# Kernel optimization log

Hardware: AMD Instinct MI355X
Metric: run time of the kernel (lower is better)

The kernel has to match this reference:

```python
import jax, jax.numpy as jnp
import numpy as np
import math

D = 128          # cfg.hiden_features_size
P0, P1 = 32, 32  # cfg.patch_size
T = 1.0          # default forward arg t


def _temporal_pe():
    # pe_k[i, :] = cat_j [sin(arg(t,i,j)), cos(arg(t,i,j))], i in [0,P1), j in [0,P0//2)
    i = jnp.arange(P1, dtype=jnp.float32)[:, None]          # [P1, 1]
    j = jnp.arange(P0 // 2, dtype=jnp.float32)[None, :]     # [1, P0//2]
    arg = T * jnp.pi * i / (1000.0 ** (2.0 * j / D))         # [P1, P0//2]
    pe = jnp.stack([jnp.sin(arg), jnp.cos(arg)], axis=-1)    # [P1, P0//2, 2]
    return pe.reshape(P1, P0)                                # [P1, P0]


def setup_inputs() -> dict:
    key = jax.random.key(0)
    kx, kw, kb = jax.random.split(key, 3)
    N, S = 128, P0 * P1
    x = jax.random.normal(kx, (N, S, D), dtype=jnp.float32)
    W = jax.random.normal(kw, (3 * D, D), dtype=jnp.float32) * (1.0 / math.sqrt(D))
    b = jax.random.normal(kb, (3 * D,), dtype=jnp.float32) * 0.01
    return {"x": x, "W": W, "b": b}


def reference(x, W, b):
    N, S, d = x.shape  # S = P0*P1, d = D
    # temporal positional encoding: multiply in spatial layout [N, P0, P1, d]
    pe = _temporal_pe()                                  # [P1, P0] (broadcast over x's [P0, P1])
    xs = x.reshape(N, P0, P1, d) * pe[None, :, :, None]
    xs = xs.reshape(N, S, d)
    # fused qkv projection: Linear(d, 3d)
    h = jnp.einsum('nsd,fd->nsf', xs, W) + b             # [N, S, 3d]
    # quirky split: view(N, S*d, 3) interleaves features in groups of 3
    qkv = h.reshape(N, S * d, 3)
    q, k, v = qkv[..., 0], qkv[..., 1], qkv[..., 2]      # each [N, S*d]
    # attention over the batch dimension: scores are [N, N]
    scores = (q @ k.T) / math.sqrt(d)
    attn = jax.nn.softmax(scores, axis=-1)
    return attn @ v                                      # [N, S*d]
```

## Files before the change

kernel.cpp:

```cpp
#include <hip/hip_runtime.h>
#include <math.h>

#define N_   128
#define S_   1024
#define D_   128
#define SD_  (S_ * D_)

#define WSP_PLANE 49152
#define NREP 16
#define SB   2
#define GRID_SC (S_ / SB)

typedef __attribute__((ext_vector_type(8))) short bf16x8;
typedef __attribute__((ext_vector_type(4))) short bf16x4;
typedef __attribute__((ext_vector_type(4))) float f32x4;
#define MFMA16 __builtin_amdgcn_mfma_f32_16x16x32_bf16

__device__ __forceinline__ float pe_scale(int s) {
    int i = s >> 5;
    int c = s & 31;
    double rexp = pow(1000.0, -(double)(c & ~1) / 128.0);
    double arg = M_PI * (double)i * rexp;
    return (float)((c & 1) ? cos(arg) : sin(arg));
}

__device__ __forceinline__ unsigned short bf16_rn(float f) {
    unsigned int u = __float_as_uint(f);
    u += 0x7fff + ((u >> 16) & 1);
    return (unsigned short)(u >> 16);
}
__device__ __forceinline__ float bf16_f(unsigned short h) {
    return __uint_as_float(((unsigned int)h) << 16);
}
__device__ __forceinline__ void split2(float f, unsigned short& h, unsigned short& l) {
    h = bf16_rn(f);
    l = bf16_rn(f - bf16_f(h));
}

__device__ __forceinline__ void load_split8(const float* p, float scale,
                                            bf16x8& hi, bf16x8& lo) {
    float4 u0 = *(const float4*)(p);
    float4 u1 = *(const float4*)(p + 4);
    unsigned short h[8], l[8];
    split2(u0.x * scale, h[0], l[0]); split2(u0.y * scale, h[1], l[1]);
    split2(u0.z * scale, h[2], l[2]); split2(u0.w * scale, h[3], l[3]);
    split2(u1.x * scale, h[4], l[4]); split2(u1.y * scale, h[5], l[5]);
    split2(u1.z * scale, h[6], l[6]); split2(u1.w * scale, h[7], l[7]);
    hi = bf16x8{(short)h[0],(short)h[1],(short)h[2],(short)h[3],
                (short)h[4],(short)h[5],(short)h[6],(short)h[7]};
    lo = bf16x8{(short)l[0],(short)l[1],(short)l[2],(short)l[3],
                (short)l[4],(short)l[5],(short)l[6],(short)l[7]};
}

__global__ __launch_bounds__(256) void k_prep(const float* __restrict__ W,
                                              unsigned short* __restrict__ Wsp,
                                              float* __restrict__ peT) {
    const int idx = blockIdx.x * 256 + threadIdx.x;
    if (idx < S_) peT[idx] = pe_scale(idx);
    const int rg = idx >> 7;
    const int d  = idx & 127;
    const int p  = rg % 3;
    const int r  = rg / 3;
    const int rc = r >> 5, m = r & 31;
    const int ks = d >> 5, quad = (d >> 3) & 3, j = d & 7;
    unsigned short h, l;
    split2(W[idx], h, l);
    const size_t off = (size_t)((((p * 4 + rc) * 4 + ks) * 4 + quad) * 32 + m) * 8 + j;
    Wsp[off] = h;
    Wsp[off + WSP_PLANE] = l;
}

__global__ __launch_bounds__(512, 4) void k_scores(const float* __restrict__ x,
                                                   const unsigned short* __restrict__ Wsp,
                                                   const float* __restrict__ b,
                                                   const float* __restrict__ peT,
                                                   float* __restrict__ sc,
                                                   int store_mode) {
    __shared__ unsigned short qk[4][128 * 40];
    __shared__ float bl[384];

    const int t    = threadIdx.x;
    const int lane = t & 63;
    const int wv   = t >> 6;
    const int lid  = lane & 15;
    const int quad = lane >> 4;

    if (t < 128) { bl[t] = b[t]; bl[t + 128] = b[t + 128]; bl[t + 256] = b[t + 256]; }
    __syncthreads();

    const f32x4 fzero = {0.f, 0.f, 0.f, 0.f};
    f32x4 sacc[8];
#pragma unroll
    for (int j = 0; j < 8; ++j) sacc[j] = fzero;

    for (int ss = 0; ss < SB; ++ss) {
        const int s = blockIdx.x * SB + ss;
        const float ps = peT[s];

        bf16x8 xh[4], xl[4];
        {
            const int row = wv * 16 + lid;
            const float* xp = x + (size_t)row * SD_ + (size_t)s * D_;
#pragma unroll
            for (int ks = 0; ks < 4; ++ks)
                load_split8(xp + ks * 32 + quad * 8, ps, xh[ks], xl[ks]);
        }

        for (int rc = 0; rc < 4; ++rc) {
            for (int p = 0; p < 2; ++p) {
                f32x4 pacc[2];
                pacc[0] = fzero; pacc[1] = fzero;
#pragma unroll
                for (int ks = 0; ks < 4; ++ks) {
                    const unsigned short* wb =
                        Wsp + (size_t)(((p * 4 + rc) * 4 + ks) * 4 + quad) * 256;
                    bf16x8 wh[2], wl[2];
#pragma unroll
                    for (int mt = 0; mt < 2; ++mt) {
                        wh[mt] = *(const bf16x8*)(wb + (mt * 16 + lid) * 8);
                        wl[mt] = *(const bf16x8*)(wb + WSP_PLANE + (mt * 16 + lid) * 8);
                    }
#pragma unroll
                    for (int mt = 0; mt < 2; ++mt) {
                        pacc[mt] = MFMA16(wh[mt], xh[ks], pacc[mt], 0, 0, 0);
                        pacc[mt] = MFMA16(wh[mt], xl[ks], pacc[mt], 0, 0, 0);
                        pacc[mt] = MFMA16(wl[mt], xh[ks], pacc[mt], 0, 0, 0);
                    }
                }
#pragma unroll
                for (int mt = 0; mt < 2; ++mt) {
                    const int n = wv * 16 + lid;
                    unsigned short hh[4], ll[4];
#pragma unroll
                    for (int r = 0; r < 4; ++r) {
                        const int rg = rc * 32 + mt * 16 + quad * 4 + r;
                        float qv = pacc[mt][r] + bl[3 * rg + p];
                        split2(qv, hh[r], ll[r]);
                    }
                    bf16x4 hv = {(short)hh[0], (short)hh[1], (short)hh[2], (short)hh[3]};
                    bf16x4 lv = {(short)ll[0], (short)ll[1], (short)ll[2], (short)ll[3]};
                    *(bf16x4*)&qk[p * 2 + 0][n * 40 + mt * 16 + quad * 4] = hv;
                    *(bf16x4*)&qk[p * 2 + 1][n * 40 + mt * 16 + quad * 4] = lv;
                }
            }
            __syncthreads();
            {
                const int row = wv * 16 + lid;
                bf16x8 qh = *(const bf16x8*)&qk[0][row * 40 + quad * 8];
                bf16x8 ql = *(const bf16x8*)&qk[1][row * 40 + quad * 8];
#pragma unroll
                for (int ntp = 0; ntp < 8; ++ntp) {
                    const int krow = ntp * 16 + lid;
                    bf16x8 kh = *(const bf16x8*)&qk[2][krow * 40 + quad * 8];
                    bf16x8 kl = *(const bf16x8*)&qk[3][krow * 40 + quad * 8];
                    sacc[ntp] = MFMA16(qh, kh, sacc[ntp], 0, 0, 0);
                    sacc[ntp] = MFMA16(qh, kl, sacc[ntp], 0, 0, 0);
                    sacc[ntp] = MFMA16(ql, kh, sacc[ntp], 0, 0, 0);
                }
            }
            __syncthreads();
        }
    }

    float* rep = sc + (store_mode ? (size_t)blockIdx.x * (N_ * N_)
                                  : (size_t)(blockIdx.x & (NREP - 1)) * (N_ * N_));
#pragma unroll
    for (int ntp = 0; ntp < 8; ++ntp)
#pragma unroll
        for (int r = 0; r < 4; ++r) {
            const int n  = wv * 16 + quad * 4 + r;
            const int np = ntp * 16 + lid;
            if (store_mode) rep[n * N_ + np] = sacc[ntp][r];
            else            atomicAdd(&rep[n * N_ + np], sacc[ntp][r]);
        }
}

__global__ __launch_bounds__(1024) void k_softmax(const float* __restrict__ sc, int R,
                                                  unsigned short* __restrict__ att2) {
    const int n  = blockIdx.x;
    const int t  = threadIdx.x;
    const int rg = t >> 5;
    const int c4 = (t & 31) * 4;

    float4 a = {0.f, 0.f, 0.f, 0.f};
    for (int rep = rg; rep < R; rep += 32) {
        const float4 p = *(const float4*)&sc[(size_t)rep * (N_ * N_) + n * N_ + c4];
        a.x += p.x; a.y += p.y; a.z += p.z; a.w += p.w;
    }
    __shared__ float tmp[32][128];
    *(float4*)&tmp[rg][c4] = a;
    __syncthreads();

    __shared__ float red[2];
    __shared__ float red2[2];

    float v = 0.f;
    if (t < 128) {
#pragma unroll
        for (int g = 0; g < 32; ++g) v += tmp[g][t];
        v *= 0.08838834764831845f;
    }

    float m = v;
#pragma unroll
    for (int o = 32; o > 0; o >>= 1) m = fmaxf(m, __shfl_xor(m, o));
    if (t < 128 && (t & 63) == 0) red[t >> 6] = m;
    __syncthreads();
    m = fmaxf(red[0], red[1]);

    float e = (t < 128) ? expf(v - m) : 0.f;
    float sum = e;
#pragma unroll
    for (int o = 32; o > 0; o >>= 1) sum += __shfl_xor(sum, o);
    if (t < 128 && (t & 63) == 0) red2[t >> 6] = sum;
    __syncthreads();
    sum = red2[0] + red2[1];

    if (t < 128) {
        const int ks = t >> 5, quad = (t >> 3) & 3, j = t & 7;
        att2[(size_t)(((ks * 4 + quad) * 128) + n) * 8 + j] = bf16_rn(e / sum);
    }
}

__global__ __launch_bounds__(256, 2) void k_out(const float* __restrict__ x,
                                                const unsigned short* __restrict__ Wsp,
                                                const float* __restrict__ b,
                                                const unsigned short* __restrict__ att2,
                                                const float* __restrict__ peT,
                                                float* __restrict__ out) {
    __shared__ unsigned short vT[128 * 136];
    __shared__ float bv[128];

    const int t    = threadIdx.x;
    const int lane = t & 63;
    const int wv   = t >> 6;
    const int lid  = lane & 15;
    const int quad = lane >> 4;
    const int s    = blockIdx.x;
    const float ps = peT[s];

    if (t < 128) bv[t] = b[3 * t + 2];
    __syncthreads();

    const f32x4 fzero = {0.f, 0.f, 0.f, 0.f};

    bf16x8 xh[2][4], xl[2][4];
#pragma unroll
    for (int mt = 0; mt < 2; ++mt) {
        const int row = (wv * 2 + mt) * 16 + lid;
        const float* xp = x + (size_t)row * SD_ + (size_t)s * D_;
#pragma unroll
        for (int ks = 0; ks < 4; ++ks)
            load_split8(xp + ks * 32 + quad * 8, ps, xh[mt][ks], xl[mt][ks]);
    }

    for (int rc = 0; rc < 4; ++rc) {
        f32x4 vacc[2][2];
        vacc[0][0] = fzero; vacc[0][1] = fzero; vacc[1][0] = fzero; vacc[1][1] = fzero;
#pragma unroll
        for (int ks = 0; ks < 4; ++ks) {
            const unsigned short* wb =
                Wsp + (size_t)(((2 * 4 + rc) * 4 + ks) * 4 + quad) * 256;
            bf16x8 wh[2], wl[2];
#pragma unroll
            for (int nt = 0; nt < 2; ++nt) {
                wh[nt] = *(const bf16x8*)(wb + (nt * 16 + lid) * 8);
                wl[nt] = *(const bf16x8*)(wb + WSP_PLANE + (nt * 16 + lid) * 8);
            }
#pragma unroll
            for (int mt = 0; mt < 2; ++mt)
#pragma unroll
                for (int nt = 0; nt < 2; ++nt) {
                    vacc[mt][nt] = MFMA16(xh[mt][ks], wh[nt], vacc[mt][nt], 0, 0, 0);
                    vacc[mt][nt] = MFMA16(xh[mt][ks], wl[nt], vacc[mt][nt], 0, 0, 0);
                    vacc[mt][nt] = MFMA16(xl[mt][ks], wh[nt], vacc[mt][nt], 0, 0, 0);
                }
        }
#pragma unroll
        for (int mt = 0; mt < 2; ++mt)
#pragma unroll
            for (int nt = 0; nt < 2; ++nt) {
                const int r = rc * 32 + nt * 16 + lid;
                const float bias = bv[r];
                unsigned short hh[4];
#pragma unroll
                for (int i = 0; i < 4; ++i) hh[i] = bf16_rn(vacc[mt][nt][i] + bias);
                bf16x4 hv = {(short)hh[0], (short)hh[1], (short)hh[2], (short)hh[3]};
                *(bf16x4*)&vT[r * 136 + (wv * 2 + mt) * 16 + quad * 4] = hv;
            }
    }
    __syncthreads();

    {
        f32x4 oacc[2][8];
#pragma unroll
        for (int i = 0; i < 2; ++i)
#pragma unroll
            for (int j = 0; j < 8; ++j) oacc[i][j] = fzero;
#pragma unroll
        for (int ks = 0; ks < 4; ++ks) {
            const int kofs = ks * 32 + quad * 8;
            bf16x8 a[2];
#pragma unroll
            for (int mt = 0; mt < 2; ++mt)
                a[mt] = *(const bf16x8*)&vT[((wv * 2 + mt) * 16 + lid) * 136 + kofs];
#pragma unroll
            for (int nt = 0; nt < 8; ++nt) {
                bf16x8 bb = *(const bf16x8*)&att2[(size_t)(((ks * 4 + quad) * 128) +
                                                           (nt * 16 + lid)) * 8];
#pragma unroll
                for (int mt = 0; mt < 2; ++mt)
                    oacc[mt][nt] = MFMA16(a[mt], bb, oacc[mt][nt], 0, 0, 0);
            }
        }
#pragma unroll
        for (int mt = 0; mt < 2; ++mt)
#pragma unroll
            for (int nt = 0; nt < 8; ++nt) {
                const int r = (wv * 2 + mt) * 16 + quad * 4;
                const int n = nt * 16 + lid;
                *(float4*)&out[(size_t)n * SD_ + (size_t)s * D_ + r] = *(float4*)&oacc[mt][nt];
            }
    }
}

extern "C" void kernel_launch(void* const* d_in, const int* in_sizes, int n_in,
                              void* d_out, int out_size, void* d_ws, size_t ws_size,
                              hipStream_t stream) {
    const float* x = (const float*)d_in[0];
    const float* W = (const float*)d_in[1];
    const float* b = (const float*)d_in[2];
    float* out = (float*)d_out;

    const size_t store_bytes = (size_t)GRID_SC * N_ * N_ * sizeof(float);
    const size_t rep_bytes   = (size_t)NREP * N_ * N_ * sizeof(float);
    const size_t tail_bytes  = (size_t)N_ * N_ * sizeof(unsigned short)
                             + (size_t)2 * WSP_PLANE * sizeof(unsigned short)
                             + (size_t)S_ * sizeof(float);
    const int store_mode = (ws_size >= store_bytes + tail_bytes) ? 1 : 0;
    const size_t sc_bytes = store_mode ? store_bytes : rep_bytes;

    float* scores        = (float*)d_ws;
    unsigned short* att2 = (unsigned short*)((char*)d_ws + sc_bytes);
    unsigned short* Wsp  = att2 + N_ * N_;
    float* peT           = (float*)(Wsp + 2 * WSP_PLANE);

    if (!store_mode)
        hipMemsetAsync(scores, 0, sc_bytes, stream);

    hipLaunchKernelGGL(k_prep,    dim3(192),     dim3(256), 0, stream, W, Wsp, peT);
    hipLaunchKernelGGL(k_scores,  dim3(GRID_SC), dim3(512), 0, stream, x, Wsp, b, peT,
                       scores, store_mode);
    hipLaunchKernelGGL(k_softmax, dim3(N_),      dim3(1024), 0, stream, scores,
                       store_mode ? GRID_SC : NREP, att2);
    hipLaunchKernelGGL(k_out,     dim3(1024),    dim3(256), 0, stream, x, Wsp, b, att2,
                       peT, out);
}
```

Measured before the change: 215.4 us.

## Fold Q·Kᵀ through precomputed Wq·Wkᵀ matrix and drop per-row constant bias terms

Rewrites the score computation as x·(Wq^T Wk)·x^T scaled by pe², precomputing M = Wq^T Wk (and u = bq·Wk) in a new small prep kernel. This halves the projection MFMA work in k_scores, since Q no longer has to be materialised, and removes one barrier per rc step by double-buffering the LDS tile. Bias terms that are constant along a softmax row are dropped, and the k-bias dot product is accumulated as an extra row that softmax adds back. It also raises NREP and adds one extra launch, which changes rounding behaviour and increases the work done in the softmax reduction.

```diff
diff --git a/kernel.cpp b/kernel.cpp
--- a/kernel.cpp
+++ b/kernel.cpp
@@ -7,9 +7,11 @@
 #define SD_  (S_ * D_)
 
 #define WSP_PLANE 49152
-#define NREP 16
+#define MSP_PLANE 16384
+#define NREP 64
 #define SB   2
 #define GRID_SC (S_ / SB)
+#define PSTRIDE ((N_ + 1) * N_)
 
 typedef __attribute__((ext_vector_type(8))) short bf16x8;
 typedef __attribute__((ext_vector_type(4))) short bf16x4;
@@ -70,14 +72,40 @@
     Wsp[off + WSP_PLANE] = l;
 }
 
+__global__ __launch_bounds__(128) void k_prepM(const float* __restrict__ W,
+                                               const float* __restrict__ b,
+                                               unsigned short* __restrict__ Msp,
+                                               float* __restrict__ uo) {
+    const int dp = blockIdx.x;
+    const int e  = threadIdx.x;
+    float acc = 0.f;
+#pragma unroll 4
+    for (int g = 0; g < 128; ++g)
+        acc += W[(3 * g) * 128 + dp] * W[(3 * g + 1) * 128 + e];
+    unsigned short h, l;
+    split2(acc, h, l);
+    const int rc = dp >> 5, m = dp & 31;
+    const int ks = e >> 5, quad = (e >> 3) & 3, j = e & 7;
+    const size_t off = (size_t)(((rc * 4 + ks) * 4 + quad) * 32 + m) * 8 + j;
+    Msp[off] = h;
+    Msp[off + MSP_PLANE] = l;
+    if (blockIdx.x == 0) {
+        float ua = 0.f;
+#pragma unroll 4
+        for (int g = 0; g < 128; ++g)
+            ua += b[3 * g] * W[(3 * g + 1) * 128 + e];
+        uo[e] = ua;
+    }
+}
+
 __global__ __launch_bounds__(512, 4) void k_scores(const float* __restrict__ x,
-                                                   const unsigned short* __restrict__ Wsp,
-                                                   const float* __restrict__ b,
+                                                   const unsigned short* __restrict__ Msp,
+                                                   const float* __restrict__ u,
                                                    const float* __restrict__ peT,
                                                    float* __restrict__ sc,
                                                    int store_mode) {
-    __shared__ unsigned short qk[4][128 * 40];
-    __shared__ float bl[384];
+    __shared__ unsigned short y2[2][2][128 * 40];
+    __shared__ float ul[128];
 
     const int t    = threadIdx.x;
     const int lane = t & 63;
@@ -85,94 +113,121 @@
     const int lid  = lane & 15;
     const int quad = lane >> 4;
 
-    if (t < 128) { bl[t] = b[t]; bl[t + 128] = b[t + 128]; bl[t + 256] = b[t + 256]; }
+    if (t < 128) ul[t] = u[t];
     __syncthreads();
 
     const f32x4 fzero = {0.f, 0.f, 0.f, 0.f};
     f32x4 sacc[8];
 #pragma unroll
     for (int j = 0; j < 8; ++j) sacc[j] = fzero;
+    float tk = 0.f;
 
     for (int ss = 0; ss < SB; ++ss) {
         const int s = blockIdx.x * SB + ss;
         const float ps = peT[s];
+        const float ps2 = ps * ps;
 
         bf16x8 xh[4], xl[4];
         {
             const int row = wv * 16 + lid;
             const float* xp = x + (size_t)row * SD_ + (size_t)s * D_;
-#pragma unroll
-            for (int ks = 0; ks < 4; ++ks)
-                load_split8(xp + ks * 32 + quad * 8, ps, xh[ks], xl[ks]);
+            float dot = 0.f;
+#pragma unroll
+            for (int ks = 0; ks < 4; ++ks) {
+                const float* pp = xp + ks * 32 + quad * 8;
+                float4 u0 = *(const float4*)pp;
+                float4 u1 = *(const float4*)(pp + 4);
+                const float* uu = &ul[ks * 32 + quad * 8];
+                dot += u0.x * uu[0] + u0.y * uu[1] + u0.z * uu[2] + u0.w * uu[3]
+                     + u1.x * uu[4] + u1.y * uu[5] + u1.z * uu[6] + u1.w * uu[7];
+                unsigned short h[8], l[8];
+                split2(u0.x, h[0], l[0]); split2(u0.y, h[1], l[1]);
+                split2(u0.z, h[2], l[2]); split2(u0.w, h[3], l[3]);
+                split2(u1.x, h[4], l[4]); split2(u1.y, h[5], l[5]);
+                split2(u1.z, h[6], l[6]); split2(u1.w, h[7], l[7]);
+                xh[ks] = bf16x8{(short)h[0],(short)h[1],(short)h[2],(short)h[3],
+                                (short)h[4],(short)h[5],(short)h[6],(short)h[7]};
+                xl[ks] = bf16x8{(short)l[0],(short)l[1],(short)l[2],(short)l[3],
+                                (short)l[4],(short)l[5],(short)l[6],(short)l[7]};
+            }
+            tk += ps * dot;
         }
 
+#pragma unroll
         for (int rc = 0; rc < 4; ++rc) {
-            for (int p = 0; p < 2; ++p) {
-                f32x4 pacc[2];
-                pacc[0] = fzero; pacc[1] = fzero;
-#pragma unroll
-                for (int ks = 0; ks < 4; ++ks) {
-                    const unsigned short* wb =
-                        Wsp + (size_t)(((p * 4 + rc) * 4 + ks) * 4 + quad) * 256;
-                    bf16x8 wh[2], wl[2];
-#pragma unroll
-                    for (int mt = 0; mt < 2; ++mt) {
-                        wh[mt] = *(const bf16x8*)(wb + (mt * 16 + lid) * 8);
-                        wl[mt] = *(const bf16x8*)(wb + WSP_PLANE + (mt * 16 + lid) * 8);
-                    }
-#pragma unroll
-                    for (int mt = 0; mt < 2; ++mt) {
-                        pacc[mt] = MFMA16(wh[mt], xh[ks], pacc[mt], 0, 0, 0);
-                        pacc[mt] = MFMA16(wh[mt], xl[ks], pacc[mt], 0, 0, 0);
-                        pacc[mt] = MFMA16(wl[mt], xh[ks], pacc[mt], 0, 0, 0);
-                    }
+            const int buf = rc & 1;
+            f32x4 pacc[2];
+            pacc[0] = fzero; pacc[1] = fzero;
+#pragma unroll
+            for (int ks = 0; ks < 4; ++ks) {
+                const unsigned short* mb =
+                    Msp + (size_t)((rc * 4 + ks) * 4 + quad) * 256;
+                bf16x8 wh[2], wl[2];
+#pragma unroll
+                for (int mt = 0; mt < 2; ++mt) {
+                    wh[mt] = *(const bf16x8*)(mb + (mt * 16 + lid) * 8);
+                    wl[mt] = *(const bf16x8*)(mb + MSP_PLANE + (mt * 16 + lid) * 8);
                 }
 #pragma unroll
                 for (int mt = 0; mt < 2; ++mt) {
-                    const int n = wv * 16 + lid;
-                    unsigned short hh[4], ll[4];
-#pragma unroll
-                    for (int r = 0; r < 4; ++r) {
-                        const int rg = rc * 32 + mt * 16 + quad * 4 + r;
-                        float qv = pacc[mt][r] + bl[3 * rg + p];
-                        split2(qv, hh[r], ll[r]);
-                    }
-                    bf16x4 hv = {(short)hh[0], (short)hh[1], (short)hh[2], (short)hh[3]};
-                    bf16x4 lv = {(short)ll[0], (short)ll[1], (short)ll[2], (short)ll[3]};
-                    *(bf16x4*)&qk[p * 2 + 0][n * 40 + mt * 16 + quad * 4] = hv;
-                    *(bf16x4*)&qk[p * 2 + 1][n * 40 + mt * 16 + quad * 4] = lv;
+                    pacc[mt] = MFMA16(wh[mt], xh[ks], pacc[mt], 0, 0, 0);
+                    pacc[mt] = MFMA16(wh[mt], xl[ks], pacc[mt], 0, 0, 0);
+                    pacc[mt] = MFMA16(wl[mt], xh[ks], pacc[mt], 0, 0, 0);
                 }
             }
+#pragma unroll
+            for (int mt = 0; mt < 2; ++mt) {
+                const int n = wv * 16 + lid;
+                unsigned short hh[4], ll[4];
+#pragma unroll
+                for (int r = 0; r < 4; ++r) {
+                    float yv = pacc[mt][r] * ps2;
+                    split2(yv, hh[r], ll[r]);
+                }
+                bf16x4 hv = {(short)hh[0], (short)hh[1], (short)hh[2], (short)hh[3]};
+                bf16x4 lv = {(short)ll[0], (short)ll[1], (short)ll[2], (short)ll[3]};
+                *(bf16x4*)&y2[buf][0][n * 40 + mt * 16 + quad * 4] = hv;
+                *(bf16x4*)&y2[buf][1][n * 40 + mt * 16 + quad * 4] = lv;
+            }
             __syncthreads();
-            {
-                const int row = wv * 16 + lid;
-                bf16x8 qh = *(const bf16x8*)&qk[0][row * 40 + quad * 8];
-                bf16x8 ql = *(const bf16x8*)&qk[1][row * 40 + quad * 8];
-#pragma unroll
-                for (int ntp = 0; ntp < 8; ++ntp) {
-                    const int krow = ntp * 16 + lid;
-                    bf16x8 kh = *(const bf16x8*)&qk[2][krow * 40 + quad * 8];
-                    bf16x8 kl = *(const bf16x8*)&qk[3][krow * 40 + quad * 8];
-                    sacc[ntp] = MFMA16(qh, kh, sacc[ntp], 0, 0, 0);
-                    sacc[ntp] = MFMA16(qh, kl, sacc[ntp], 0, 0, 0);
-                    sacc[ntp] = MFMA16(ql, kh, sacc[ntp], 0, 0, 0);
-                }
-            }
-            __syncthreads();
+#pragma unroll
+            for (int ntp = 0; ntp < 8; ++ntp) {
+                const int yrow = ntp * 16 + lid;
+                bf16x8 yh = *(const bf16x8*)&y2[buf][0][yrow * 40 + quad * 8];
+                bf16x8 yl = *(const bf16x8*)&y2[buf][1][yrow * 40 + quad * 8];
+                sacc[ntp] = MFMA16(xh[rc], yh, sacc[ntp], 0, 0, 0);
+                sacc[ntp] = MFMA16(xh[rc], yl, sacc[ntp], 0, 0, 0);
+                sacc[ntp] = MFMA16(xl[rc], yh, sacc[ntp], 0, 0, 0);
+            }
         }
     }
 
-    float* rep = sc + (store_mode ? (size_t)blockIdx.x * (N_ * N_)
-                                  : (size_t)(blockIdx.x & (NREP - 1)) * (N_ * N_));
-#pragma unroll
-    for (int ntp = 0; ntp < 8; ++ntp)
-#pragma unroll
-        for (int r = 0; r < 4; ++r) {
-            const int n  = wv * 16 + quad * 4 + r;
-            const int np = ntp * 16 + lid;
-            if (store_mode) rep[n * N_ + np] = sacc[ntp][r];
-            else            atomicAdd(&rep[n * N_ + np], sacc[ntp][r]);
-        }
+    tk += __shfl_xor(tk, 16);
+    tk += __shfl_xor(tk, 32);
+
+    float* rep = sc + (size_t)(store_mode ? blockIdx.x
+                                          : (blockIdx.x & (NREP - 1))) * PSTRIDE;
+    if (store_mode) {
+#pragma unroll
+        for (int ntp = 0; ntp < 8; ++ntp)
+#pragma unroll
+            for (int r = 0; r < 4; ++r) {
+                const int n  = wv * 16 + quad * 4 + r;
+                const int np = ntp * 16 + lid;
+                rep[n * N_ + np] = sacc[ntp][r];
+            }
+        if (quad == 0) rep[N_ * N_ + wv * 16 + lid] = tk;
+    } else {
+#pragma unroll
+        for (int ntp = 0; ntp < 8; ++ntp)
+#pragma unroll
+            for (int r = 0; r < 4; ++r) {
+                const int n  = wv * 16 + quad * 4 + r;
+                const int np = ntp * 16 + lid;
+                atomicAdd(&rep[n * N_ + np], sacc[ntp][r]);
+            }
+        if (quad == 0) atomicAdd(&rep[N_ * N_ + wv * 16 + lid], tk);
+    }
 }
 
 __global__ __launch_bounds__(1024) void k_softmax(const float* __restrict__ sc, int R,
@@ -182,13 +237,19 @@
     const int rg = t >> 5;
     const int c4 = (t & 31) * 4;
 
-    float4 a = {0.f, 0.f, 0.f, 0.f};
+    float4 a  = {0.f, 0.f, 0.f, 0.f};
+    float4 tk = {0.f, 0.f, 0.f, 0.f};
     for (int rep = rg; rep < R; rep += 32) {
-        const float4 p = *(const float4*)&sc[(size_t)rep * (N_ * N_) + n * N_ + c4];
+        const size_t base = (size_t)rep * PSTRIDE;
+        const float4 p = *(const float4*)&sc[base + n * N_ + c4];
         a.x += p.x; a.y += p.y; a.z += p.z; a.w += p.w;
+        const float4 q = *(const float4*)&sc[base + N_ * N_ + c4];
+        tk.x += q.x; tk.y += q.y; tk.z += q.z; tk.w += q.w;
     }
     __shared__ float tmp[32][128];
-    *(float4*)&tmp[rg][c4] = a;
+    __shared__ float tmp2[32][128];
+    *(float4*)&tmp[rg][c4]  = a;
+    *(float4*)&tmp2[rg][c4] = tk;
     __syncthreads();
 
     __shared__ float red[2];
@@ -196,9 +257,10 @@
 
     float v = 0.f;
     if (t < 128) {
-#pragma unroll
-        for (int g = 0; g < 32; ++g) v += tmp[g][t];
-        v *= 0.08838834764831845f;
+        float q = 0.f, k = 0.f;
+#pragma unroll
+        for (int g = 0; g < 32; ++g) { q += tmp[g][t]; k += tmp2[g][t]; }
+        v = (q + k) * 0.08838834764831845f;
     }
 
     float m = v;
@@ -332,11 +394,13 @@
     const float* b = (const float*)d_in[2];
     float* out = (float*)d_out;
 
-    const size_t store_bytes = (size_t)GRID_SC * N_ * N_ * sizeof(float);
-    const size_t rep_bytes   = (size_t)NREP * N_ * N_ * sizeof(float);
+    const size_t store_bytes = (size_t)GRID_SC * PSTRIDE * sizeof(float);
+    const size_t rep_bytes   = (size_t)NREP * PSTRIDE * sizeof(float);
     const size_t tail_bytes  = (size_t)N_ * N_ * sizeof(unsigned short)
                              + (size_t)2 * WSP_PLANE * sizeof(unsigned short)
-                             + (size_t)S_ * sizeof(float);
+                             + (size_t)S_ * sizeof(float)
+                             + (size_t)2 * MSP_PLANE * sizeof(unsigned short)
+                             + (size_t)N_ * sizeof(float);
     const int store_mode = (ws_size >= store_bytes + tail_bytes) ? 1 : 0;
     const size_t sc_bytes = store_mode ? store_bytes : rep_bytes;
 
@@ -344,15 +408,18 @@
     unsigned short* att2 = (unsigned short*)((char*)d_ws + sc_bytes);
     unsigned short* Wsp  = att2 + N_ * N_;
     float* peT           = (float*)(Wsp + 2 * WSP_PLANE);
+    unsigned short* Msp  = (unsigned short*)(peT + S_);
+    float* uvec          = (float*)(Msp + 2 * MSP_PLANE);
 
     if (!store_mode)
         hipMemsetAsync(scores, 0, sc_bytes, stream);
 
-    hipLaunchKernelGGL(k_prep,    dim3(192),     dim3(256), 0, stream, W, Wsp, peT);
-    hipLaunchKernelGGL(k_scores,  dim3(GRID_SC), dim3(512), 0, stream, x, Wsp, b, peT,
+    hipLaunchKernelGGL(k_prep,    dim3(192),     dim3(256),  0, stream, W, Wsp, peT);
+    hipLaunchKernelGGL(k_prepM,   dim3(128),     dim3(128),  0, stream, W, b, Msp, uvec);
+    hipLaunchKernelGGL(k_scores,  dim3(GRID_SC), dim3(512),  0, stream, x, Msp, uvec, peT,
                        scores, store_mode);
     hipLaunchKernelGGL(k_softmax, dim3(N_),      dim3(1024), 0, stream, scores,
                        store_mode ? GRID_SC : NREP, att2);
-    hipLaunchKernelGGL(k_out,     dim3(1024),    dim3(256), 0, stream, x, Wsp, b, att2,
+    hipLaunchKernelGGL(k_out,     dim3(1024),    dim3(256),  0, stream, x, Wsp, b, att2,
                        peT, out);
 }
```

Measured after the change: 399.8 us. 1.86x slower.
